# Optimization experiments

Measured on AMD Instinct MI355X. Metric: run time of the kernel, lower is better.

Reference implementation:

```python
import jax, jax.numpy as jnp
import numpy as np

DT = 0.02        # time step
DT_SKIP = DT * 20
ITERS = 49       # BDF2 iterations hardcoded in forward()
P = 64           # tronc (reduced dim)
NG_U = 8000      # HR sample count, u-equation
NG_V = 8000      # HR sample count, v-equation
B = 32           # batch of trajectories


def setup_inputs() -> dict:
    key = jax.random.key(0)
    k0, k1, k2, k3, k4 = jax.random.split(key, 5)
    state = jax.random.normal(k0, (B, P), dtype=jnp.float32)
    Ap = jax.random.normal(k1, (P, P), dtype=jnp.float32) * 0.05
    W_all_u = jax.random.normal(k2, (4 * NG_U, P), dtype=jnp.float32) * 0.02
    W_all_v = jax.random.normal(k3, (4 * NG_V, P), dtype=jnp.float32) * 0.02
    P_proj = jax.random.normal(k4, (P, NG_U + NG_V), dtype=jnp.float32) * 0.02
    return {"state": state, "Ap": Ap, "W_all_u": W_all_u,
            "W_all_v": W_all_v, "P_proj": P_proj}


def _rhs(a, W_all_u, W_all_v, P_proj):
    # a: (B, p) -> (B, p). Batched hyper-reduced quadratic RHS.
    zu = a @ W_all_u.T                       # (B, 4*Ng_u)
    uu, vu, dxu, dyu = jnp.split(zu, 4, axis=1)
    fu = uu * dxu + vu * dyu                 # (B, Ng_u)
    zv = a @ W_all_v.T                       # (B, 4*Ng_v)
    uv, vv, dxv, dyv = jnp.split(zv, 4, axis=1)
    fv = uv * dxv + vv * dyv                 # (B, Ng_v)
    concat = jnp.concatenate([fu, fv], axis=1)  # (B, Ng_u+Ng_v)
    return -(concat @ P_proj.T)              # (B, p)


def reference(state, Ap, W_all_u, W_all_v, P_proj):
    dt = jnp.float32(DT)
    a0 = state[:, :P]                        # state_rom (B, p)
    eye = jnp.eye(P, dtype=state.dtype)
    mat_1st = eye - dt * Ap[:P, :P]          # I - dt*A
    mat_2nd = 3.0 * eye - 2.0 * dt * Ap[:P, :P]

    # first step: implicit Euler
    f0 = _rhs(a0, W_all_u, W_all_v, P_proj)
    r0 = a0 + dt * f0
    a1 = jnp.linalg.solve(mat_1st, r0.T).T   # == lu_solve(LU_1st, ...)

    # BDF2 recurrence
    def step(carry, _):
        a_prev, f_prev, a_new = carry
        f_new = _rhs(a_new, W_all_u, W_all_v, P_proj)
        r = 4.0 * a_new - a_prev + 4.0 * dt * f_new - 2.0 * dt * f_prev
        a_next = jnp.linalg.solve(mat_2nd, r.T).T
        return (a_new, f_new, a_next), None

    (_, _, out_new), _ = jax.lax.scan(step, (a0, f0, a1), None, length=ITERS)
    return (out_new - a0) / jnp.float32(DT_SKIP)
```

## Files before the change

### kernel.cpp

```cpp
#include <hip/hip_runtime.h>

#define DTC 0.02f
#define INV_DT_SKIP 2.5f
#define NBLK 64
#define NSTEP 50
#define NACT 500

typedef __attribute__((ext_vector_type(8))) __bf16 bf16x8;
typedef __attribute__((ext_vector_type(4))) float f32x4;
typedef __attribute__((ext_vector_type(8))) unsigned short us8;
typedef unsigned long long u64t;

__device__ inline unsigned short f2bf(float x) {
    unsigned u = __float_as_uint(x);
    unsigned r = u + 0x7FFF + ((u >> 16) & 1u);
    return (unsigned short)(r >> 16);
}
__device__ inline float bf2f(unsigned short h) {
    return __uint_as_float(((unsigned)h) << 16);
}
__device__ inline unsigned pack2(float a, float b) {
    return (unsigned)f2bf(a) | ((unsigned)f2bf(b) << 16);
}
__device__ inline void gstore32(unsigned* p, unsigned v) {
    __hip_atomic_store(p, v, __ATOMIC_RELAXED, __HIP_MEMORY_SCOPE_AGENT);
}
__device__ inline u64t gload64(const u64t* p) {
    return __hip_atomic_load(p, __ATOMIC_RELAXED, __HIP_MEMORY_SCOPE_AGENT);
}
__device__ inline void gstore64(u64t* p, u64t v) {
    __hip_atomic_store(p, v, __ATOMIC_RELAXED, __HIP_MEMORY_SCOPE_AGENT);
}

__global__ __launch_bounds__(256) void kinv(const float* __restrict__ Ap,
                                            float* __restrict__ inv1,
                                            float* __restrict__ inv2) {
    const int t = threadIdx.x;
    const float coef  = (blockIdx.x == 0) ? DTC : (2.0f * DTC / 3.0f);
    const float scale = (blockIdx.x == 0) ? 1.0f : (1.0f / 3.0f);
    float* outp = (blockIdx.x == 0) ? inv1 : inv2;

    __shared__ float ET[64 * 68];
    __shared__ float XA[64 * 68];
    __shared__ float XB[64 * 68];

    for (int idx = t; idx < 4096; idx += 256) {
        int r = idx >> 6, c = idx & 63;
        float e = coef * Ap[idx];
        ET[c * 68 + r] = e;
        XA[r * 68 + c] = ((r == c) ? 1.0f : 0.0f) + e;
    }
    __syncthreads();

    const int rr = (t >> 4) << 2;
    const int cc = (t & 15) << 2;
    float* bufs[2] = {XA, XB};
    for (int it = 0; it < 3; it++) {
        const float* Xin = bufs[it & 1];
        float* Xout = bufs[(it + 1) & 1];
        float acc[4][4];
        #pragma unroll
        for (int i = 0; i < 4; i++)
            #pragma unroll
            for (int j = 0; j < 4; j++)
                acc[i][j] = ((rr + i) == (cc + j)) ? 1.0f : 0.0f;
        for (int k = 0; k < 64; k++) {
            float4 e4 = *(const float4*)&ET[k * 68 + rr];
            float4 x4 = *(const float4*)&Xin[k * 68 + cc];
            float ev[4] = {e4.x, e4.y, e4.z, e4.w};
            float xv[4] = {x4.x, x4.y, x4.z, x4.w};
            #pragma unroll
            for (int i = 0; i < 4; i++)
                #pragma unroll
                for (int j = 0; j < 4; j++)
                    acc[i][j] += ev[i] * xv[j];
        }
        __syncthreads();
        #pragma unroll
        for (int i = 0; i < 4; i++)
            #pragma unroll
            for (int j = 0; j < 4; j++)
                Xout[(rr + i) * 68 + cc + j] = acc[i][j];
        __syncthreads();
    }
    const float* Xf = bufs[1];
    for (int idx = t; idx < 4096; idx += 256) {
        int r = idx >> 6, c = idx & 63;
        outp[idx] = scale * Xf[r * 68 + c];
    }
}

__global__ void kzero(unsigned* __restrict__ cnt) {
    if (threadIdx.x == 0) *cnt = 0u;
}

__device__ inline void gridbar(unsigned* cnt, unsigned target) {
    __syncthreads();
    if (threadIdx.x == 0) {
        __hip_atomic_fetch_add(cnt, 1u, __ATOMIC_RELEASE, __HIP_MEMORY_SCOPE_AGENT);
        while (__hip_atomic_load(cnt, __ATOMIC_ACQUIRE, __HIP_MEMORY_SCOPE_AGENT) < target)
            __builtin_amdgcn_s_sleep(4);
    }
    __syncthreads();
}

__global__ __launch_bounds__(512, 2)
void kmain(const float* __restrict__ state,
           const float* __restrict__ Wu,
           const float* __restrict__ Wv,
           const float* __restrict__ Pp,
           const float* __restrict__ inv1,
           const float* __restrict__ inv2,
           unsigned* __restrict__ pbuf,
           u64t* __restrict__ fg,
           unsigned* __restrict__ cnt,
           float* __restrict__ out) {
    const int t = threadIdx.x;
    const int l = t & 63;
    const int w = t >> 6;
    const int blk = blockIdx.x;
    const int q = blk * 8 + w;
    const bool active = (q < NACT);

    __shared__ float Ab[3][2176];
    __shared__ float fb[8][2][16][36];
    __shared__ float red[8][1024];
    __shared__ float fpp[2][2048];
    __shared__ float rbuf[32 * 68];

    for (int i = t; i < 2048; i += 512) Ab[0][(i >> 6) * 68 + (i & 63)] = state[i];
    for (int i = t; i < 8192; i += 512) ((float*)red)[i] = 0.f;

    const int nr = l & 15;
    const int c0 = (l >> 4) << 3;
    const float* W = (q < 250) ? Wu : Wv;
    const int gl0 = ((q < 250) ? q : q - 250) * 32;

    bf16x8 wf[2][4][2], pf[4], sf[4][2];
    if (active) {
        #pragma unroll
        for (int th = 0; th < 2; th++)
            #pragma unroll
            for (int rb = 0; rb < 4; rb++)
                #pragma unroll
                for (int kt = 0; kt < 2; kt++) {
                    const float* s = W + (size_t)(rb * 8000 + gl0 + th * 16 + nr) * 64 + kt * 32 + c0;
                    us8 o;
                    #pragma unroll
                    for (int j = 0; j < 8; j++) o[j] = f2bf(s[j]);
                    wf[th][rb][kt] = __builtin_bit_cast(bf16x8, o);
                }
        #pragma unroll
        for (int pt = 0; pt < 4; pt++) {
            const float* s = Pp + (size_t)(pt * 16 + nr) * 16000 + q * 32 + c0;
            us8 o;
            #pragma unroll
            for (int j = 0; j < 8; j++) o[j] = f2bf(s[j]);
            pf[pt] = __builtin_bit_cast(bf16x8, o);
        }
    }
    if (w < 2) {
        #pragma unroll
        for (int pt = 0; pt < 4; pt++)
            #pragma unroll
            for (int kt = 0; kt < 2; kt++) {
                int p = pt * 16 + nr;
                const float* s = inv2 + (size_t)p * 64 + kt * 32 + c0;
                us8 o;
                #pragma unroll
                for (int j = 0; j < 8; j++) {
                    float v = s[j] - ((p == kt * 32 + c0 + j) ? (1.0f / 3.0f) : 0.0f);
                    o[j] = f2bf(v);
                }
                sf[pt][kt] = __builtin_bit_cast(bf16x8, o);
            }
    }
    __syncthreads();

    int ia_prev = 2, ia_cur = 0, ia_next = 1;
    int ifc = 0;

    for (int k = 0; k < NSTEP; k++) {
        if (active) {
            bf16x8 ahi[2][2], alo[2][2];
            const float* ac = Ab[ia_cur];
            #pragma unroll
            for (int mt = 0; mt < 2; mt++)
                #pragma unroll
                for (int kt = 0; kt < 2; kt++) {
                    us8 hv, lv;
                    #pragma unroll
                    for (int j = 0; j < 8; j++) {
                        float x = ac[(mt * 16 + nr) * 68 + kt * 32 + c0 + j];
                        unsigned short h = f2bf(x);
                        hv[j] = h;
                        lv[j] = f2bf(x - bf2f(h));
                    }
                    ahi[mt][kt] = __builtin_bit_cast(bf16x8, hv);
                    alo[mt][kt] = __builtin_bit_cast(bf16x8, lv);
                }
            const int col = l & 15, q4 = l >> 4;
            #pragma unroll
            for (int mt = 0; mt < 2; mt++)
                #pragma unroll
                for (int th = 0; th < 2; th++) {
                    f32x4 z[4];
                    #pragma unroll
                    for (int rb = 0; rb < 4; rb++) {
                        f32x4 acc = {0.f, 0.f, 0.f, 0.f};
                        #pragma unroll
                        for (int kt = 0; kt < 2; kt++) {
                            acc = __builtin_amdgcn_mfma_f32_16x16x32_bf16(ahi[mt][kt], wf[th][rb][kt], acc, 0, 0, 0);
                            acc = __builtin_amdgcn_mfma_f32_16x16x32_bf16(alo[mt][kt], wf[th][rb][kt], acc, 0, 0, 0);
                        }
                        z[rb] = acc;
                    }
                    #pragma unroll
                    for (int r = 0; r < 4; r++) {
                        float f = z[0][r] * z[2][r] + z[1][r] * z[3][r];
                        fb[w][mt][q4 * 4 + r][th * 16 + col] = f;
                    }
                }
        }
        __syncthreads();

        bf16x8 ff[2];
        if (active) {
            #pragma unroll
            for (int mt = 0; mt < 2; mt++) {
                us8 fv;
                #pragma unroll
                for (int j = 0; j < 8; j++) fv[j] = f2bf(fb[w][mt][nr][c0 + j]);
                ff[mt] = __builtin_bit_cast(bf16x8, fv);
            }
        }

        #pragma unroll
        for (int mt = 0; mt < 2; mt++) {
            if (active) {
                const int col = l & 15, q4 = l >> 4;
                #pragma unroll
                for (int pt = 0; pt < 4; pt++) {
                    f32x4 rc = {0.f, 0.f, 0.f, 0.f};
                    rc = __builtin_amdgcn_mfma_f32_16x16x32_bf16(ff[mt], pf[pt], rc, 0, 0, 0);
                    #pragma unroll
                    for (int r = 0; r < 4; r++)
                        red[w][(q4 * 4 + r) * 64 + pt * 16 + col] = rc[r];
                }
            }
            __syncthreads();
            {
                float s0 = 0.f, s1 = 0.f;
                #pragma unroll
                for (int w8 = 0; w8 < 8; w8++) {
                    s0 += red[w8][2 * t];
                    s1 += red[w8][2 * t + 1];
                }
                gstore32(&pbuf[blk * 1024 + mt * 512 + t], pack2(s0, s1));
            }
            __syncthreads();
        }

        gridbar(cnt, (unsigned)(NBLK * (2 * k + 1)));

        {
            u64t v = gload64((const u64t*)pbuf + (size_t)l * 512 + blk * 8 + w);
            float s0 = bf2f((unsigned short)(v & 0xffff));
            float s1 = bf2f((unsigned short)((v >> 16) & 0xffff));
            float s2 = bf2f((unsigned short)((v >> 32) & 0xffff));
            float s3 = bf2f((unsigned short)(v >> 48));
            #pragma unroll
            for (int off = 32; off >= 1; off >>= 1) {
                s0 += __shfl_down(s0, off);
                s1 += __shfl_down(s1, off);
                s2 += __shfl_down(s2, off);
                s3 += __shfl_down(s3, off);
            }
            if (l == 0) {
                u64t pv = (u64t)pack2(-s0, -s1) | ((u64t)pack2(-s2, -s3) << 32);
                gstore64(&fg[blk * 8 + w], pv);
            }
        }

        gridbar(cnt, (unsigned)(NBLK * (2 * k + 2)));

        {
            u64t v = gload64(&fg[t]);
            float fv[4] = { bf2f((unsigned short)(v & 0xffff)),
                            bf2f((unsigned short)((v >> 16) & 0xffff)),
                            bf2f((unsigned short)((v >> 32) & 0xffff)),
                            bf2f((unsigned short)(v >> 48)) };
            const int b = (4 * t) >> 6, p0 = (4 * t) & 63;
            float* fc = fpp[ifc];
            const float* fp = fpp[ifc ^ 1];
            #pragma unroll
            for (int jj = 0; jj < 4; jj++) {
                int i = 4 * t + jj;
                float f = fv[jj];
                fc[i] = f;
                int row = b * 68 + p0 + jj;
                float av = Ab[ia_cur][row];
                float rv = (k == 0) ? (av + DTC * f)
                                    : (4.f * av - Ab[ia_prev][row]
                                       + 4.f * DTC * f - 2.f * DTC * fp[i]);
                rbuf[row] = rv;
            }
        }
        __syncthreads();

        if (w < 2) {
            auto solve = [&](const bf16x8 (&S)[4][2], float cbase) {
                int m = w * 16 + nr;
                bf16x8 rhi[2], rlo[2];
                #pragma unroll
                for (int kt = 0; kt < 2; kt++) {
                    us8 hv, lv;
                    #pragma unroll
                    for (int j = 0; j < 8; j++) {
                        float x = rbuf[m * 68 + kt * 32 + c0 + j];
                        unsigned short h = f2bf(x);
                        hv[j] = h;
                        lv[j] = f2bf(x - bf2f(h));
                    }
                    rhi[kt] = __builtin_bit_cast(bf16x8, hv);
                    rlo[kt] = __builtin_bit_cast(bf16x8, lv);
                }
                int col = l & 15, q4 = l >> 4;
                #pragma unroll
                for (int pt = 0; pt < 4; pt++) {
                    f32x4 acc;
                    #pragma unroll
                    for (int r = 0; r < 4; r++)
                        acc[r] = rbuf[(w * 16 + q4 * 4 + r) * 68 + pt * 16 + col] * cbase;
                    #pragma unroll
                    for (int kt = 0; kt < 2; kt++) {
                        acc = __builtin_amdgcn_mfma_f32_16x16x32_bf16(rhi[kt], S[pt][kt], acc, 0, 0, 0);
                        acc = __builtin_amdgcn_mfma_f32_16x16x32_bf16(rlo[kt], S[pt][kt], acc, 0, 0, 0);
                    }
                    #pragma unroll
                    for (int r = 0; r < 4; r++)
                        Ab[ia_next][(w * 16 + q4 * 4 + r) * 68 + pt * 16 + col] = acc[r];
                }
            };
            if (k == 0) {
                bf16x8 s1f[4][2];
                #pragma unroll
                for (int pt = 0; pt < 4; pt++)
                    #pragma unroll
                    for (int kt = 0; kt < 2; kt++) {
                        int p = pt * 16 + nr;
                        const float* s = inv1 + (size_t)p * 64 + kt * 32 + c0;
                        us8 o;
                        #pragma unroll
                        for (int j = 0; j < 8; j++) {
                            float v = s[j] - ((p == kt * 32 + c0 + j) ? 1.0f : 0.0f);
                            o[j] = f2bf(v);
                        }
                        s1f[pt][kt] = __builtin_bit_cast(bf16x8, o);
                    }
                solve(s1f, 1.0f);
            } else {
                solve(sf, 1.0f / 3.0f);
            }
        }
        __syncthreads();

        if (k == NSTEP - 1 && blk == 0) {
            for (int i = t; i < 2048; i += 512)
                out[i] = (Ab[ia_next][(i >> 6) * 68 + (i & 63)] - state[i]) * INV_DT_SKIP;
        }

        int tmp = ia_prev; ia_prev = ia_cur; ia_cur = ia_next; ia_next = tmp;
        ifc ^= 1;
    }
}

extern "C" void kernel_launch(void* const* d_in, const int* in_sizes, int n_in,
                              void* d_out, int out_size, void* d_ws, size_t ws_size,
                              hipStream_t stream) {
    const float* state = (const float*)d_in[0];
    const float* Ap    = (const float*)d_in[1];
    const float* Wu    = (const float*)d_in[2];
    const float* Wv    = (const float*)d_in[3];
    const float* Pp    = (const float*)d_in[4];
    float* out = (float*)d_out;
    float* ws  = (float*)d_ws;

    float* inv1 = ws;
    float* inv2 = ws + 4096;
    unsigned* cnt = (unsigned*)(ws + 8192);
    u64t* fg = (u64t*)(ws + 8192 + 16);
    unsigned* pbuf = (unsigned*)(ws + 8192 + 16 + 1024);

    hipLaunchKernelGGL(kzero, dim3(1), dim3(64), 0, stream, cnt);
    hipLaunchKernelGGL(kinv, dim3(2), dim3(256), 0, stream, Ap, inv1, inv2);
    hipLaunchKernelGGL(kmain, dim3(NBLK), dim3(512), 0, stream,
                       state, Wu, Wv, Pp, inv1, inv2, pbuf, fg, cnt, out);
}
```

Before: 620.7 us.

## Replace two atomic-counter grid barriers per step with one per-block flag barrier

Each step's two grid barriers (reduce-scatter, then broadcast of f) become a single barrier. After it, every block redundantly reduces all 64 blocks' partial sums itself. The barrier changes from a contended fetch-add counter to per-block monotonic flags polled by one wavefront, and pbuf is double-buffered by step parity so the next step's writes cannot overwrite data still being read. The previous f is now kept in registers rather than shared memory. The trade is more global-load traffic per block (64 partial slices each) in exchange for one fewer grid-wide synchronisation per step.

Result: slower. 656.1 us (+5.7%).

```diff
diff --git a/kernel.cpp b/kernel.cpp
--- a/kernel.cpp
+++ b/kernel.cpp
@@ -25,11 +25,11 @@
 __device__ inline void gstore32(unsigned* p, unsigned v) {
     __hip_atomic_store(p, v, __ATOMIC_RELAXED, __HIP_MEMORY_SCOPE_AGENT);
 }
+__device__ inline unsigned gload32(const unsigned* p) {
+    return __hip_atomic_load(p, __ATOMIC_RELAXED, __HIP_MEMORY_SCOPE_AGENT);
+}
 __device__ inline u64t gload64(const u64t* p) {
     return __hip_atomic_load(p, __ATOMIC_RELAXED, __HIP_MEMORY_SCOPE_AGENT);
-}
-__device__ inline void gstore64(u64t* p, u64t v) {
-    __hip_atomic_store(p, v, __ATOMIC_RELAXED, __HIP_MEMORY_SCOPE_AGENT);
 }
 
 __global__ __launch_bounds__(256) void kinv(const float* __restrict__ Ap,
@@ -90,16 +90,21 @@
     }
 }
 
-__global__ void kzero(unsigned* __restrict__ cnt) {
-    if (threadIdx.x == 0) *cnt = 0u;
-}
-
-__device__ inline void gridbar(unsigned* cnt, unsigned target) {
+__global__ void kzero(unsigned* __restrict__ flags) {
+    if (threadIdx.x < NBLK) flags[threadIdx.x] = 0u;
+}
+
+__device__ inline void flagbar(unsigned* flags, int blk, unsigned target) {
     __syncthreads();
-    if (threadIdx.x == 0) {
-        __hip_atomic_fetch_add(cnt, 1u, __ATOMIC_RELEASE, __HIP_MEMORY_SCOPE_AGENT);
-        while (__hip_atomic_load(cnt, __ATOMIC_ACQUIRE, __HIP_MEMORY_SCOPE_AGENT) < target)
-            __builtin_amdgcn_s_sleep(4);
+    if (threadIdx.x < 64) {
+        if (threadIdx.x == 0)
+            __hip_atomic_store(&flags[blk], target, __ATOMIC_RELEASE, __HIP_MEMORY_SCOPE_AGENT);
+        for (;;) {
+            unsigned v = __hip_atomic_load(&flags[threadIdx.x], __ATOMIC_ACQUIRE,
+                                           __HIP_MEMORY_SCOPE_AGENT);
+            if (__all(v >= target)) break;
+            __builtin_amdgcn_s_sleep(2);
+        }
     }
     __syncthreads();
 }
@@ -112,8 +117,7 @@
            const float* __restrict__ inv1,
            const float* __restrict__ inv2,
            unsigned* __restrict__ pbuf,
-           u64t* __restrict__ fg,
-           unsigned* __restrict__ cnt,
+           unsigned* __restrict__ flags,
            float* __restrict__ out) {
     const int t = threadIdx.x;
     const int l = t & 63;
@@ -125,7 +129,6 @@
     __shared__ float Ab[3][2176];
     __shared__ float fb[8][2][16][36];
     __shared__ float red[8][1024];
-    __shared__ float fpp[2][2048];
     __shared__ float rbuf[32 * 68];
 
     for (int i = t; i < 2048; i += 512) Ab[0][(i >> 6) * 68 + (i & 63)] = state[i];
@@ -178,9 +181,12 @@
     __syncthreads();
 
     int ia_prev = 2, ia_cur = 0, ia_next = 1;
-    int ifc = 0;
+    float fprev[4];
 
     for (int k = 0; k < NSTEP; k++) {
+        const int par = k & 1;
+        unsigned* pslot = pbuf + (size_t)par * (NBLK * 1024) + blk * 1024;
+
         if (active) {
             bf16x8 ahi[2][2], alo[2][2];
             const float* ac = Ab[ia_cur];
@@ -256,54 +262,41 @@
                     s0 += red[w8][2 * t];
                     s1 += red[w8][2 * t + 1];
                 }
-                gstore32(&pbuf[blk * 1024 + mt * 512 + t], pack2(s0, s1));
+                gstore32(&pslot[mt * 512 + t], pack2(s0, s1));
             }
             __syncthreads();
         }
 
-        gridbar(cnt, (unsigned)(NBLK * (2 * k + 1)));
-
+        flagbar(flags, blk, (unsigned)(k + 1));
+
+        float fv[4];
         {
-            u64t v = gload64((const u64t*)pbuf + (size_t)l * 512 + blk * 8 + w);
-            float s0 = bf2f((unsigned short)(v & 0xffff));
-            float s1 = bf2f((unsigned short)((v >> 16) & 0xffff));
-            float s2 = bf2f((unsigned short)((v >> 32) & 0xffff));
-            float s3 = bf2f((unsigned short)(v >> 48));
-            #pragma unroll
-            for (int off = 32; off >= 1; off >>= 1) {
-                s0 += __shfl_down(s0, off);
-                s1 += __shfl_down(s1, off);
-                s2 += __shfl_down(s2, off);
-                s3 += __shfl_down(s3, off);
-            }
-            if (l == 0) {
-                u64t pv = (u64t)pack2(-s0, -s1) | ((u64t)pack2(-s2, -s3) << 32);
-                gstore64(&fg[blk * 8 + w], pv);
-            }
-        }
-
-        gridbar(cnt, (unsigned)(NBLK * (2 * k + 2)));
+            const u64t* pb = (const u64t*)(pbuf + (size_t)par * (NBLK * 1024));
+            float s0 = 0.f, s1 = 0.f, s2 = 0.f, s3 = 0.f;
+            #pragma unroll 8
+            for (int s = 0; s < NBLK; s++) {
+                u64t v = gload64(pb + (size_t)s * 512 + t);
+                unsigned lo = (unsigned)v, hi = (unsigned)(v >> 32);
+                s0 += __uint_as_float(lo << 16);
+                s1 += __uint_as_float(lo & 0xffff0000u);
+                s2 += __uint_as_float(hi << 16);
+                s3 += __uint_as_float(hi & 0xffff0000u);
+            }
+            fv[0] = -s0; fv[1] = -s1; fv[2] = -s2; fv[3] = -s3;
+        }
 
         {
-            u64t v = gload64(&fg[t]);
-            float fv[4] = { bf2f((unsigned short)(v & 0xffff)),
-                            bf2f((unsigned short)((v >> 16) & 0xffff)),
-                            bf2f((unsigned short)((v >> 32) & 0xffff)),
-                            bf2f((unsigned short)(v >> 48)) };
             const int b = (4 * t) >> 6, p0 = (4 * t) & 63;
-            float* fc = fpp[ifc];
-            const float* fp = fpp[ifc ^ 1];
             #pragma unroll
             for (int jj = 0; jj < 4; jj++) {
-                int i = 4 * t + jj;
                 float f = fv[jj];
-                fc[i] = f;
                 int row = b * 68 + p0 + jj;
                 float av = Ab[ia_cur][row];
                 float rv = (k == 0) ? (av + DTC * f)
                                     : (4.f * av - Ab[ia_prev][row]
-                                       + 4.f * DTC * f - 2.f * DTC * fp[i]);
+                                       + 4.f * DTC * f - 2.f * DTC * fprev[jj]);
                 rbuf[row] = rv;
+                fprev[jj] = f;
             }
         }
         __syncthreads();
@@ -371,7 +364,6 @@
         }
 
         int tmp = ia_prev; ia_prev = ia_cur; ia_cur = ia_next; ia_next = tmp;
-        ifc ^= 1;
     }
 }
 
@@ -388,12 +380,11 @@
 
     float* inv1 = ws;
     float* inv2 = ws + 4096;
-    unsigned* cnt = (unsigned*)(ws + 8192);
-    u64t* fg = (u64t*)(ws + 8192 + 16);
-    unsigned* pbuf = (unsigned*)(ws + 8192 + 16 + 1024);
-
-    hipLaunchKernelGGL(kzero, dim3(1), dim3(64), 0, stream, cnt);
+    unsigned* flags = (unsigned*)(ws + 8192);
+    unsigned* pbuf  = (unsigned*)(ws + 8192 + 64);
+
+    hipLaunchKernelGGL(kzero, dim3(1), dim3(64), 0, stream, flags);
     hipLaunchKernelGGL(kinv, dim3(2), dim3(256), 0, stream, Ap, inv1, inv2);
     hipLaunchKernelGGL(kmain, dim3(NBLK), dim3(512), 0, stream,
-                       state, Wu, Wv, Pp, inv1, inv2, pbuf, fg, cnt, out);
-}
+                       state, Wu, Wv, Pp, inv1, inv2, pbuf, flags, out);
+}
```
